# Performance work log

Measured on AMD Instinct MI355X. Metric: run time of the kernel, lower is better.

The kernel has to match this reference:

```python
import jax, jax.numpy as jnp
import numpy as np

B, SENSORY, STATE, MOTOR = 4096, 64, 128, 32
ODE_UNFOLDS = 6
EPS = 1e-8
ELAPSED_TIME = 1.0


def setup_inputs() -> dict:
    key = jax.random.key(0)
    ks = jax.random.split(key, 20)
    u = lambda k, shape, lo, hi: jax.random.uniform(k, shape, jnp.float32, lo, hi)
    sign = lambda k, shape: jnp.where(jax.random.bernoulli(k, 0.5, shape), 1.0, -1.0).astype(jnp.float32)
    mask = lambda k, shape: (jax.random.uniform(k, shape) < 0.75).astype(jnp.float32)
    return {
        "inputs": jax.random.normal(ks[0], (B, SENSORY), jnp.float32),
        "states": jax.random.normal(ks[1], (B, STATE), jnp.float32),
        "gleak": u(ks[2], (STATE,), 0.001, 1.0),
        "vleak": u(ks[3], (STATE,), -0.2, 0.2),
        "cm": u(ks[4], (STATE,), 0.4, 0.6),
        "w": u(ks[5], (STATE, STATE), 0.001, 1.0),
        "sigma": u(ks[6], (STATE, STATE), 3.0, 8.0),
        "mu": u(ks[7], (STATE, STATE), 0.3, 0.8),
        "erev": sign(ks[8], (STATE, STATE)),
        "sensory_w": u(ks[9], (SENSORY, STATE), 0.001, 1.0),
        "sensory_sigma": u(ks[10], (SENSORY, STATE), 3.0, 8.0),
        "sensory_mu": u(ks[11], (SENSORY, STATE), 0.3, 0.8),
        "sensory_erev": sign(ks[12], (SENSORY, STATE)),
        "sparsity_mask": mask(ks[13], (STATE, STATE)),
        "sensory_sparsity_mask": mask(ks[14], (SENSORY, STATE)),
        "input_w": jnp.ones((SENSORY,), jnp.float32),
        "input_b": jnp.zeros((SENSORY,), jnp.float32),
        "output_w": jnp.ones((MOTOR,), jnp.float32),
        "output_b": jnp.zeros((MOTOR,), jnp.float32),
    }


def _syn_sigmoid(v_pre, mu, sigma):
    # v_pre: [B, P] -> [B, P, 1]; mu/sigma: [P, S]
    return jax.nn.sigmoid(sigma * (v_pre[..., None] - mu))


def reference(inputs, states, gleak, vleak, cm, w, sigma, mu, erev,
              sensory_w, sensory_sigma, sensory_mu, sensory_erev,
              sparsity_mask, sensory_sparsity_mask,
              input_w, input_b, output_w, output_b):
    # input mapping (affine); make_positive_fn = Identity (explicit constraints)
    x = inputs * input_w + input_b

    # sensory contributions (computed once, shared across unfolds)
    sens_act = sensory_w * _syn_sigmoid(x, sensory_mu, sensory_sigma)  # [B, In, S]
    sens_act = sens_act * sensory_sparsity_mask
    w_num_sensory = jnp.sum(sens_act * sensory_erev, axis=1)  # [B, S]
    w_den_sensory = jnp.sum(sens_act, axis=1)                 # [B, S]

    cm_t = cm / (ELAPSED_TIME / ODE_UNFOLDS)  # [S]

    v_pre = states
    for _ in range(ODE_UNFOLDS):
        w_act = w * _syn_sigmoid(v_pre, mu, sigma)   # [B, S, S]
        w_act = w_act * sparsity_mask
        w_numerator = jnp.sum(w_act * erev, axis=1) + w_num_sensory
        w_denominator = jnp.sum(w_act, axis=1) + w_den_sensory
        numerator = cm_t * v_pre + gleak * vleak + w_numerator
        denominator = cm_t + gleak + w_denominator
        v_pre = numerator / (denominator + EPS)

    # output mapping: slice motor neurons, then affine
    output = v_pre[:, :MOTOR] * output_w + output_b
    return output, v_pre
```

## Files before the change

kernel.cpp:

```cpp
#include <hip/hip_runtime.h>

#define LOG2E 1.4426950408889634f

constexpr int Bsz = 4096, Ssz = 128, Isz = 64, MOTOR = 32;
constexpr int BT = 8, R = 4, NT = 256;

__global__ void ltc_prep(const float* __restrict__ w, const float* __restrict__ sigma,
                         const float* __restrict__ mu, const float* __restrict__ erev,
                         const float* __restrict__ smask,
                         const float* __restrict__ sw, const float* __restrict__ ssig,
                         const float* __restrict__ smu, const float* __restrict__ serev,
                         const float* __restrict__ ssmask,
                         float2* __restrict__ AB, float* __restrict__ WE,
                         float2* __restrict__ ABs, float* __restrict__ WEs)
{
  int idx = blockIdx.x * blockDim.x + threadIdx.x;
  if (idx < Ssz * Ssz) {
    float wp = w[idx] * smask[idx];
    WE[idx] = wp * erev[idx];
    float sg = sigma[idx];
    AB[idx] = make_float2(-sg * LOG2E, sg * mu[idx] * LOG2E);
  } else if (idx < Ssz * Ssz + Isz * Ssz) {
    int k = idx - Ssz * Ssz;
    float wp = sw[k] * ssmask[k];
    WEs[k] = wp * serev[k];
    float sg = ssig[k];
    ABs[k] = make_float2(-sg * LOG2E, sg * smu[k] * LOG2E);
  }
}

__launch_bounds__(NT)
__global__ void ltc_main(const float* __restrict__ inputs, const float* __restrict__ states,
                         const float* __restrict__ gleak, const float* __restrict__ vleak,
                         const float* __restrict__ cmv,
                         const float* __restrict__ iw, const float* __restrict__ ib,
                         const float* __restrict__ ow, const float* __restrict__ ob,
                         const float2* __restrict__ AB, const float* __restrict__ WE,
                         const float2* __restrict__ ABs, const float* __restrict__ WEs,
                         float* __restrict__ out)
{
  __shared__ float vsh[BT][Ssz];
  __shared__ float xsh[BT][Isz];
  const int t = threadIdx.x;
  const int s = t & (Ssz - 1);
  const int g = t >> 7;
  const int b0 = blockIdx.x * BT;
  const int r0 = g * R;

  for (int k = t; k < BT * Isz; k += NT) {
    int r = k >> 6, i = k & (Isz - 1);
    xsh[r][i] = inputs[(b0 + r) * Isz + i] * iw[i] + ib[i];
  }
  for (int k = t; k < BT * Ssz; k += NT) {
    int r = k >> 7, ss = k & (Ssz - 1);
    vsh[r][ss] = states[(b0 + r) * Ssz + ss];
  }
  const float cmt = cmv[s] * 6.0f;
  const float gl = gleak[s];
  const float gv = gl * vleak[s];
  __syncthreads();

  float sn[R], sd[R];
  #pragma unroll
  for (int r = 0; r < R; ++r) { sn[r] = 0.f; sd[r] = 0.f; }
  {
    float2 abc[4]; float wec[4];
    #pragma unroll
    for (int jj = 0; jj < 4; ++jj) { abc[jj] = ABs[jj * Ssz + s]; wec[jj] = WEs[jj * Ssz + s]; }
    for (int i4 = 0; i4 < Isz; i4 += 4) {
      float xv[R][4];
      #pragma unroll
      for (int r = 0; r < R; ++r) {
        float4 xt = *(const float4*)&xsh[r0 + r][i4];
        xv[r][0] = xt.x; xv[r][1] = xt.y; xv[r][2] = xt.z; xv[r][3] = xt.w;
      }
      float2 abn[4] = {}; float wen[4] = {};
      if (i4 + 4 < Isz) {
        #pragma unroll
        for (int jj = 0; jj < 4; ++jj) { abn[jj] = ABs[(i4 + 4 + jj) * Ssz + s]; wen[jj] = WEs[(i4 + 4 + jj) * Ssz + s]; }
      }
      #pragma unroll
      for (int jj = 0; jj < 4; ++jj) {
        #pragma unroll
        for (int r = 0; r < R; ++r) {
          float arg = fmaf(abc[jj].x, xv[r][jj], abc[jj].y);
          float u = __builtin_amdgcn_exp2f(arg);
          float sig = __builtin_amdgcn_rcpf(1.0f + u);
          sn[r] = fmaf(wec[jj], sig, sn[r]);
          sd[r] = fmaf(fabsf(wec[jj]), sig, sd[r]);
        }
      }
      #pragma unroll
      for (int jj = 0; jj < 4; ++jj) { abc[jj] = abn[jj]; wec[jj] = wen[jj]; }
    }
  }

  float vnew[R];
  for (int it = 0; it < 6; ++it) {
    float num[R], den[R];
    #pragma unroll
    for (int r = 0; r < R; ++r) { num[r] = sn[r]; den[r] = sd[r]; }
    float2 abc[4]; float wec[4];
    #pragma unroll
    for (int jj = 0; jj < 4; ++jj) { abc[jj] = AB[jj * Ssz + s]; wec[jj] = WE[jj * Ssz + s]; }
    for (int j4 = 0; j4 < Ssz; j4 += 4) {
      float vv[R][4];
      #pragma unroll
      for (int r = 0; r < R; ++r) {
        float4 vt = *(const float4*)&vsh[r0 + r][j4];
        vv[r][0] = vt.x; vv[r][1] = vt.y; vv[r][2] = vt.z; vv[r][3] = vt.w;
      }
      float2 abn[4] = {}; float wen[4] = {};
      if (j4 + 4 < Ssz) {
        #pragma unroll
        for (int jj = 0; jj < 4; ++jj) { abn[jj] = AB[(j4 + 4 + jj) * Ssz + s]; wen[jj] = WE[(j4 + 4 + jj) * Ssz + s]; }
      }
      #pragma unroll
      for (int jj = 0; jj < 4; ++jj) {
        #pragma unroll
        for (int r = 0; r < R; ++r) {
          float arg = fmaf(abc[jj].x, vv[r][jj], abc[jj].y);
          float u = __builtin_amdgcn_exp2f(arg);
          float sig = __builtin_amdgcn_rcpf(1.0f + u);
          num[r] = fmaf(wec[jj], sig, num[r]);
          den[r] = fmaf(fabsf(wec[jj]), sig, den[r]);
        }
      }
      #pragma unroll
      for (int jj = 0; jj < 4; ++jj) { abc[jj] = abn[jj]; wec[jj] = wen[jj]; }
    }
    #pragma unroll
    for (int r = 0; r < R; ++r) {
      float vo = vsh[r0 + r][s];
      float nn = fmaf(cmt, vo, gv) + num[r];
      float dd = cmt + gl + den[r];
      vnew[r] = nn / (dd + 1e-8f);
    }
    __syncthreads();
    #pragma unroll
    for (int r = 0; r < R; ++r) vsh[r0 + r][s] = vnew[r];
    __syncthreads();
  }

  #pragma unroll
  for (int r = 0; r < R; ++r) {
    int b = b0 + r0 + r;
    out[Bsz * MOTOR + b * Ssz + s] = vnew[r];
    if (s < MOTOR) out[b * MOTOR + s] = fmaf(vnew[r], ow[s], ob[s]);
  }
}

extern "C" void kernel_launch(void* const* d_in, const int* in_sizes, int n_in,
                              void* d_out, int out_size, void* d_ws, size_t ws_size,
                              hipStream_t stream) {
  const float* inputs = (const float*)d_in[0];
  const float* states = (const float*)d_in[1];
  const float* gleak  = (const float*)d_in[2];
  const float* vleak  = (const float*)d_in[3];
  const float* cmv    = (const float*)d_in[4];
  const float* w      = (const float*)d_in[5];
  const float* sigma  = (const float*)d_in[6];
  const float* mu     = (const float*)d_in[7];
  const float* erev   = (const float*)d_in[8];
  const float* sw     = (const float*)d_in[9];
  const float* ssig   = (const float*)d_in[10];
  const float* smu    = (const float*)d_in[11];
  const float* serev  = (const float*)d_in[12];
  const float* smask  = (const float*)d_in[13];
  const float* ssmask = (const float*)d_in[14];
  const float* iw     = (const float*)d_in[15];
  const float* ib     = (const float*)d_in[16];
  const float* ow     = (const float*)d_in[17];
  const float* ob     = (const float*)d_in[18];

  char* ws = (char*)d_ws;
  float2* AB  = (float2*)ws;
  float*  WE  = (float*)(ws + 131072);
  float2* ABs = (float2*)(ws + 196608);
  float*  WEs = (float*)(ws + 262144);
  float* out = (float*)d_out;

  ltc_prep<<<(Ssz * Ssz + Isz * Ssz + 255) / 256, 256, 0, stream>>>(
      w, sigma, mu, erev, smask, sw, ssig, smu, serev, ssmask, AB, WE, ABs, WEs);
  ltc_main<<<Bsz / BT, NT, 0, stream>>>(
      inputs, states, gleak, vleak, cmv, iw, ib, ow, ob, AB, WE, ABs, WEs, out);
}
```

Before: 127.6 us.

## Split presynaptic reduction across two thread halves and pack parameters as float4

Doubles the block to 512 threads, so each half of the block sums over half of the presynaptic neurons. The two halves combine their partial numerators and denominators through shared memory before the state update. The parameter tables are re-laid out in the prep kernel as interleaved float4 arrays (A, B, W) so each thread fetches four rows with one vector load. The division is also replaced by a hardware reciprocal multiply. This adds parallelism and latency hiding per block in exchange for extra shared-memory traffic, more work per barrier, and the loss of the explicit software prefetch.

```diff
diff --git a/kernel.cpp b/kernel.cpp
--- a/kernel.cpp
+++ b/kernel.cpp
@@ -3,7 +3,7 @@
 #define LOG2E 1.4426950408889634f
 
 constexpr int Bsz = 4096, Ssz = 128, Isz = 64, MOTOR = 32;
-constexpr int BT = 8, R = 4, NT = 256;
+constexpr int BT = 8, R = 4, NT = 512;
 
 __global__ void ltc_prep(const float* __restrict__ w, const float* __restrict__ sigma,
                          const float* __restrict__ mu, const float* __restrict__ erev,
@@ -11,21 +11,35 @@
                          const float* __restrict__ sw, const float* __restrict__ ssig,
                          const float* __restrict__ smu, const float* __restrict__ serev,
                          const float* __restrict__ ssmask,
-                         float2* __restrict__ AB, float* __restrict__ WE,
-                         float2* __restrict__ ABs, float* __restrict__ WEs)
+                         float4* __restrict__ A4, float4* __restrict__ B4, float4* __restrict__ W4,
+                         float4* __restrict__ A4s, float4* __restrict__ B4s, float4* __restrict__ W4s)
 {
   int idx = blockIdx.x * blockDim.x + threadIdx.x;
-  if (idx < Ssz * Ssz) {
-    float wp = w[idx] * smask[idx];
-    WE[idx] = wp * erev[idx];
-    float sg = sigma[idx];
-    AB[idx] = make_float2(-sg * LOG2E, sg * mu[idx] * LOG2E);
-  } else if (idx < Ssz * Ssz + Isz * Ssz) {
-    int k = idx - Ssz * Ssz;
-    float wp = sw[k] * ssmask[k];
-    WEs[k] = wp * serev[k];
-    float sg = ssig[k];
-    ABs[k] = make_float2(-sg * LOG2E, sg * smu[k] * LOG2E);
+  if (idx < (Ssz / 4) * Ssz) {
+    int j4 = idx >> 7, s = idx & 127;
+    float4 a, b, wv;
+    #pragma unroll
+    for (int jj = 0; jj < 4; ++jj) {
+      int e = (j4 * 4 + jj) * Ssz + s;
+      float sg = sigma[e];
+      (&a.x)[jj] = -sg * LOG2E;
+      (&b.x)[jj] = sg * mu[e] * LOG2E;
+      (&wv.x)[jj] = w[e] * smask[e] * erev[e];
+    }
+    A4[idx] = a; B4[idx] = b; W4[idx] = wv;
+  } else if (idx < (Ssz / 4) * Ssz + (Isz / 4) * Ssz) {
+    int k = idx - (Ssz / 4) * Ssz;
+    int i4 = k >> 7, s = k & 127;
+    float4 a, b, wv;
+    #pragma unroll
+    for (int jj = 0; jj < 4; ++jj) {
+      int e = (i4 * 4 + jj) * Ssz + s;
+      float sg = ssig[e];
+      (&a.x)[jj] = -sg * LOG2E;
+      (&b.x)[jj] = sg * smu[e] * LOG2E;
+      (&wv.x)[jj] = sw[e] * ssmask[e] * serev[e];
+    }
+    A4s[k] = a; B4s[k] = b; W4s[k] = wv;
   }
 }
 
@@ -35,24 +49,30 @@
                          const float* __restrict__ cmv,
                          const float* __restrict__ iw, const float* __restrict__ ib,
                          const float* __restrict__ ow, const float* __restrict__ ob,
-                         const float2* __restrict__ AB, const float* __restrict__ WE,
-                         const float2* __restrict__ ABs, const float* __restrict__ WEs,
+                         const float4* __restrict__ A4, const float4* __restrict__ B4,
+                         const float4* __restrict__ W4,
+                         const float4* __restrict__ A4s, const float4* __restrict__ B4s,
+                         const float4* __restrict__ W4s,
                          float* __restrict__ out)
 {
   __shared__ float vsh[BT][Ssz];
   __shared__ float xsh[BT][Isz];
+  __shared__ float redn[2][2][R][Ssz];
+  __shared__ float redd[2][2][R][Ssz];
+
   const int t = threadIdx.x;
-  const int s = t & (Ssz - 1);
-  const int g = t >> 7;
+  const int s = t & 127;
+  const int jh = (t >> 7) & 1;
+  const int g = t >> 8;
+  const int r0 = g * R;
   const int b0 = blockIdx.x * BT;
-  const int r0 = g * R;
 
   for (int k = t; k < BT * Isz; k += NT) {
-    int r = k >> 6, i = k & (Isz - 1);
+    int r = k >> 6, i = k & 63;
     xsh[r][i] = inputs[(b0 + r) * Isz + i] * iw[i] + ib[i];
   }
   for (int k = t; k < BT * Ssz; k += NT) {
-    int r = k >> 7, ss = k & (Ssz - 1);
+    int r = k >> 7, ss = k & 127;
     vsh[r][ss] = states[(b0 + r) * Ssz + ss];
   }
   const float cmt = cmv[s] * 6.0f;
@@ -60,93 +80,94 @@
   const float gv = gl * vleak[s];
   __syncthreads();
 
-  float sn[R], sd[R];
-  #pragma unroll
-  for (int r = 0; r < R; ++r) { sn[r] = 0.f; sd[r] = 0.f; }
+  float sn[R] = {0.f, 0.f, 0.f, 0.f}, sd[R] = {0.f, 0.f, 0.f, 0.f};
   {
-    float2 abc[4]; float wec[4];
-    #pragma unroll
-    for (int jj = 0; jj < 4; ++jj) { abc[jj] = ABs[jj * Ssz + s]; wec[jj] = WEs[jj * Ssz + s]; }
-    for (int i4 = 0; i4 < Isz; i4 += 4) {
+    const int qb = jh * (Isz / 8);
+    for (int q = 0; q < Isz / 8; ++q) {
+      int iq = qb + q;
+      float4 a4 = A4s[iq * Ssz + s];
+      float4 b4 = B4s[iq * Ssz + s];
+      float4 w4 = W4s[iq * Ssz + s];
       float xv[R][4];
       #pragma unroll
       for (int r = 0; r < R; ++r) {
-        float4 xt = *(const float4*)&xsh[r0 + r][i4];
+        float4 xt = *(const float4*)&xsh[r0 + r][iq * 4];
         xv[r][0] = xt.x; xv[r][1] = xt.y; xv[r][2] = xt.z; xv[r][3] = xt.w;
       }
-      float2 abn[4] = {}; float wen[4] = {};
-      if (i4 + 4 < Isz) {
-        #pragma unroll
-        for (int jj = 0; jj < 4; ++jj) { abn[jj] = ABs[(i4 + 4 + jj) * Ssz + s]; wen[jj] = WEs[(i4 + 4 + jj) * Ssz + s]; }
-      }
       #pragma unroll
       for (int jj = 0; jj < 4; ++jj) {
+        float av = (&a4.x)[jj], bv = (&b4.x)[jj], wv = (&w4.x)[jj];
         #pragma unroll
         for (int r = 0; r < R; ++r) {
-          float arg = fmaf(abc[jj].x, xv[r][jj], abc[jj].y);
+          float arg = fmaf(av, xv[r][jj], bv);
           float u = __builtin_amdgcn_exp2f(arg);
           float sig = __builtin_amdgcn_rcpf(1.0f + u);
-          sn[r] = fmaf(wec[jj], sig, sn[r]);
-          sd[r] = fmaf(fabsf(wec[jj]), sig, sd[r]);
+          sn[r] = fmaf(wv, sig, sn[r]);
+          sd[r] = fmaf(fabsf(wv), sig, sd[r]);
         }
       }
-      #pragma unroll
-      for (int jj = 0; jj < 4; ++jj) { abc[jj] = abn[jj]; wec[jj] = wen[jj]; }
     }
   }
 
   float vnew[R];
   for (int it = 0; it < 6; ++it) {
-    float num[R], den[R];
+    float num[R], den[R], vo[R];
     #pragma unroll
     for (int r = 0; r < R; ++r) { num[r] = sn[r]; den[r] = sd[r]; }
-    float2 abc[4]; float wec[4];
-    #pragma unroll
-    for (int jj = 0; jj < 4; ++jj) { abc[jj] = AB[jj * Ssz + s]; wec[jj] = WE[jj * Ssz + s]; }
-    for (int j4 = 0; j4 < Ssz; j4 += 4) {
+    const int qb = jh * (Ssz / 8);
+    for (int q = 0; q < Ssz / 8; ++q) {
+      int jq = qb + q;
+      float4 a4 = A4[jq * Ssz + s];
+      float4 b4 = B4[jq * Ssz + s];
+      float4 w4 = W4[jq * Ssz + s];
       float vv[R][4];
       #pragma unroll
       for (int r = 0; r < R; ++r) {
-        float4 vt = *(const float4*)&vsh[r0 + r][j4];
+        float4 vt = *(const float4*)&vsh[r0 + r][jq * 4];
         vv[r][0] = vt.x; vv[r][1] = vt.y; vv[r][2] = vt.z; vv[r][3] = vt.w;
       }
-      float2 abn[4] = {}; float wen[4] = {};
-      if (j4 + 4 < Ssz) {
-        #pragma unroll
-        for (int jj = 0; jj < 4; ++jj) { abn[jj] = AB[(j4 + 4 + jj) * Ssz + s]; wen[jj] = WE[(j4 + 4 + jj) * Ssz + s]; }
-      }
       #pragma unroll
       for (int jj = 0; jj < 4; ++jj) {
+        float av = (&a4.x)[jj], bv = (&b4.x)[jj], wv = (&w4.x)[jj];
         #pragma unroll
         for (int r = 0; r < R; ++r) {
-          float arg = fmaf(abc[jj].x, vv[r][jj], abc[jj].y);
+          float arg = fmaf(av, vv[r][jj], bv);
           float u = __builtin_amdgcn_exp2f(arg);
           float sig = __builtin_amdgcn_rcpf(1.0f + u);
-          num[r] = fmaf(wec[jj], sig, num[r]);
-          den[r] = fmaf(fabsf(wec[jj]), sig, den[r]);
+          num[r] = fmaf(wv, sig, num[r]);
+          den[r] = fmaf(fabsf(wv), sig, den[r]);
         }
       }
-      #pragma unroll
-      for (int jj = 0; jj < 4; ++jj) { abc[jj] = abn[jj]; wec[jj] = wen[jj]; }
     }
     #pragma unroll
     for (int r = 0; r < R; ++r) {
-      float vo = vsh[r0 + r][s];
-      float nn = fmaf(cmt, vo, gv) + num[r];
-      float dd = cmt + gl + den[r];
-      vnew[r] = nn / (dd + 1e-8f);
+      vo[r] = vsh[r0 + r][s];
+      redn[jh][g][r][s] = num[r];
+      redd[jh][g][r][s] = den[r];
     }
     __syncthreads();
     #pragma unroll
-    for (int r = 0; r < R; ++r) vsh[r0 + r][s] = vnew[r];
+    for (int r = 0; r < R; ++r) {
+      float fn = num[r] + redn[1 - jh][g][r][s];
+      float fd = den[r] + redd[1 - jh][g][r][s];
+      float nn = fmaf(cmt, vo[r], gv) + fn;
+      float dd = cmt + gl + fd + 1e-8f;
+      vnew[r] = nn * __builtin_amdgcn_rcpf(dd);
+    }
+    if (jh == 0) {
+      #pragma unroll
+      for (int r = 0; r < R; ++r) vsh[r0 + r][s] = vnew[r];
+    }
     __syncthreads();
   }
 
-  #pragma unroll
-  for (int r = 0; r < R; ++r) {
-    int b = b0 + r0 + r;
-    out[Bsz * MOTOR + b * Ssz + s] = vnew[r];
-    if (s < MOTOR) out[b * MOTOR + s] = fmaf(vnew[r], ow[s], ob[s]);
+  if (jh == 0) {
+    #pragma unroll
+    for (int r = 0; r < R; ++r) {
+      int b = b0 + r0 + r;
+      out[Bsz * MOTOR + b * Ssz + s] = vnew[r];
+      if (s < MOTOR) out[b * MOTOR + s] = fmaf(vnew[r], ow[s], ob[s]);
+    }
   }
 }
 
@@ -174,14 +195,17 @@
   const float* ob     = (const float*)d_in[18];
 
   char* ws = (char*)d_ws;
-  float2* AB  = (float2*)ws;
-  float*  WE  = (float*)(ws + 131072);
-  float2* ABs = (float2*)(ws + 196608);
-  float*  WEs = (float*)(ws + 262144);
+  float4* A4  = (float4*)(ws);
+  float4* B4  = (float4*)(ws + 65536);
+  float4* W4  = (float4*)(ws + 131072);
+  float4* A4s = (float4*)(ws + 196608);
+  float4* B4s = (float4*)(ws + 229376);
+  float4* W4s = (float4*)(ws + 262144);
   float* out = (float*)d_out;
 
-  ltc_prep<<<(Ssz * Ssz + Isz * Ssz + 255) / 256, 256, 0, stream>>>(
-      w, sigma, mu, erev, smask, sw, ssig, smu, serev, ssmask, AB, WE, ABs, WEs);
+  constexpr int prep_items = (Ssz / 4) * Ssz + (Isz / 4) * Ssz;
+  ltc_prep<<<(prep_items + 255) / 256, 256, 0, stream>>>(
+      w, sigma, mu, erev, smask, sw, ssig, smu, serev, ssmask, A4, B4, W4, A4s, B4s, W4s);
   ltc_main<<<Bsz / BT, NT, 0, stream>>>(
-      inputs, states, gleak, vleak, cmv, iw, ib, ow, ob, AB, WE, ABs, WEs, out);
+      inputs, states, gleak, vleak, cmv, iw, ib, ow, ob, A4, B4, W4, A4s, B4s, W4s, out);
 }
```

Result: faster. 124.8 us (-2.2%).
